# Optimization experiments

Measured on AMD Instinct MI355X. Metric: run time of the kernel, lower is better.

Reference implementation:

```python
import jax, jax.numpy as jnp
import numpy as np

H, W = 480, 640
TREF = 1.0        # reference timestamp (events warped to end of window)
TS_SCALING = 1.0  # width of timestamp normalization window
# 4 bilinear corner offsets (dy, dx): top-left, top-right, bottom-left, bottom-right
OFFS = np.array([[0.0, 0.0], [0.0, 1.0], [1.0, 0.0], [1.0, 1.0]], dtype=np.float32)


def setup_inputs() -> dict:
    key = jax.random.key(0)
    k1, k2, k3, k4, k5 = jax.random.split(key, 5)
    B, N = 4, 300000
    flow = jax.random.normal(k1, (B, 2, H, W), jnp.float32) * 2.0  # (x, y) flow maps
    ts = jax.random.uniform(k2, (B, N, 1), jnp.float32)            # event timestamps in [0,1]
    ev_y = jax.random.randint(k3, (B, N), 0, H)
    ev_x = jax.random.randint(k4, (B, N), 0, W)
    pol = jax.random.randint(k5, (B, N), 0, 2)                     # 1 = positive, 0 = negative
    return {"flow": flow, "ts": ts, "ev_y": ev_y, "ev_x": ev_x, "pol": pol}


def _corners(ev):
    """ev: [B,N,2] float (y,x) -> idx [B,4,N,2] corner coords, w [B,4,N] bilinear weights.
    Mirrors get_interpolation(): 4 integer corners, weights clamp(1-|d|,0,1) per axis."""
    base = jnp.floor(ev)[:, None, :, :]                      # [B,1,N,2]
    idx = base + jnp.asarray(OFFS)[None, :, None, :]          # [B,4,N,2]
    w = jnp.prod(jnp.clip(1.0 - jnp.abs(ev[:, None, :, :] - idx), 0.0, 1.0), axis=-1)
    return idx, w


def _splat(idx, w, pol_mask):
    """Mirrors interpolate(): masked bilinear scatter-add into a [B,1,H,W] image.
    idx: [B,4,N,2], w: [B,4,N], pol_mask: [B,1,N] (broadcast over 4 corners)."""
    B = idx.shape[0]
    inb = ((idx[..., 0] >= 0) & (idx[..., 0] <= H - 1) &
           (idx[..., 1] >= 0) & (idx[..., 1] <= W - 1)).astype(w.dtype)
    iy = jnp.clip(idx[..., 0], 0, H - 1).astype(jnp.int32)
    ix = jnp.clip(idx[..., 1], 0, W - 1).astype(jnp.int32)
    flat = (iy * W + ix).reshape(B, -1)                       # [B,4N]
    vals = (w * pol_mask * inb).reshape(B, -1)                # [B,4N]
    img = jnp.zeros((B, H * W), w.dtype).at[jnp.arange(B)[:, None], flat].add(vals)
    return img.reshape(B, 1, H, W)


def _sample(fmap, locs):
    """Mirrors get_event_flow(): bilinear gather of fmap [B,H,W] at float locs [B,N,2] (y,x)."""
    B = fmap.shape[0]
    idx, w = _corners(locs)
    inb = ((idx[..., 0] >= 0) & (idx[..., 0] <= H - 1) &
           (idx[..., 1] >= 0) & (idx[..., 1] <= W - 1)).astype(w.dtype)
    iy = jnp.clip(idx[..., 0], 0, H - 1).astype(jnp.int32)
    ix = jnp.clip(idx[..., 1], 0, W - 1).astype(jnp.int32)
    vals = fmap[jnp.arange(B)[:, None, None], iy, ix] * w * inb   # [B,4,N]
    return vals.sum(axis=1)                                        # [B,N]


def reference(flow, ts, ev_y, ev_x, pol):
    # event pixel locations (y, x)
    loc = jnp.stack([ev_y.astype(flow.dtype), ev_x.astype(flow.dtype)], axis=-1)  # [B,N,2]
    # gather per-event flow (flow channel 0 = x, channel 1 = y)
    fx = _sample(flow[:, 0], loc)   # [B,N]
    fy = _sample(flow[:, 1], loc)   # [B,N]
    # linear forward warp to tref
    dt = TREF - ts[..., 0]                                           # [B,N]
    warped = loc + dt[..., None] * jnp.stack([fy, fx], axis=-1)      # [B,N,2] (y,x)
    # iwe_formatting: bilinear splat of counts and normalized timestamps per polarity
    idx, w = _corners(warped)
    norm_ts = 1.0 - jnp.abs(TREF - ts[..., 0]) / TS_SCALING          # [B,N]
    pm_pos = (pol == 1).astype(w.dtype)[:, None, :]                  # [B,1,N]
    pm_neg = (pol == 0).astype(w.dtype)[:, None, :]
    iwe_pos = _splat(idx, w, pm_pos)
    iwe_neg = _splat(idx, w, pm_neg)
    wt = w * norm_ts[:, None, :]
    iwe_pos_ts = _splat(idx, wt, pm_pos)
    iwe_neg_ts = _splat(idx, wt, pm_neg)
    # [B,4,H,W]: (iwe_pos, iwe_neg, iwe_pos_ts, iwe_neg_ts)
    return jnp.concatenate([iwe_pos, iwe_neg, iwe_pos_ts, iwe_neg_ts], axis=1)
```

## Files before the change

kernel.cpp:

```cpp
#include <hip/hip_runtime.h>


#define IMG_H 480
#define IMG_W 640

#define OT_H 16
#define OT_W 32
#define OTY (IMG_H / OT_H)
#define OTX (IMG_W / OT_W)
#define OT_PER_B (OTY * OTX)
#define NB 4
#define NT (NB * OT_PER_B)

#define ACC_PLANE (OT_H * OT_W)

#define SCURS_STRIDE 16
#define WS_SCURS 0
#define WS_DCURS 153600
#define WS_SPILLCNT 163200
#define WS_SPILL 163840
#define SPILL_CAP 32768
#define WS_RECS 688128

#define SSORT_THREADS 512
#define K1_IPT 2
#define K1_CHUNK (SSORT_THREADS * K1_IPT)

#define Q20 1048576.0f
#define INV_Q20 9.5367431640625e-07f

__device__ __forceinline__ void
warp_from(const float* __restrict__ flow, int b, int y, int x, float t,
          float& wy, float& wx, float& nts) {
    const float* fb = flow + (size_t)b * 2 * IMG_H * IMG_W;
    const int pix = y * IMG_W + x;
    const float fx = fb[pix];
    const float fy = fb[IMG_H * IMG_W + pix];
    const float dt = 1.0f - t;
    wy = (float)y + dt * fy;
    wx = (float)x + dt * fx;
    nts = 1.0f - fabsf(1.0f - t);
}

__global__ void __launch_bounds__(SSORT_THREADS)
ssort_kernel(const float* __restrict__ flow, const float* __restrict__ ts,
             const int* __restrict__ ev_y, const int* __restrict__ ev_x,
             const int* __restrict__ pol,
             unsigned* __restrict__ scurs, unsigned* __restrict__ spillcnt,
             float4* __restrict__ spill, uint2* __restrict__ srecs,
             int N, int cap) {
    __shared__ unsigned lh[OT_PER_B];
    __shared__ unsigned lbase[OT_PER_B];
    const int tid = threadIdx.x;
    const int b = blockIdx.y;
    const int base = blockIdx.x * K1_CHUNK;

    for (int j = tid; j < OT_PER_B; j += SSORT_THREADS) lh[j] = 0;
    __syncthreads();

    unsigned mK[K1_IPT], ltK[K1_IPT], rkK[K1_IPT];
    float tsK[K1_IPT];

    #pragma unroll
    for (int k = 0; k < K1_IPT; ++k) {
        const int idx = base + k * SSORT_THREADS + tid;
        unsigned lt = 0xFFFFu, rk = 0, m = 0; float t = 0.f;
        if (idx < N) {
            const int i = b * N + idx;
            const int y = ev_y[i];
            const int x = ev_x[i];
            t = ts[i];
            const int p = pol[i];
            lt = (unsigned)((y >> 4) * OTX + (x >> 5));
            rk = atomicAdd(&lh[lt], 1u);
            m = (unsigned)y | ((unsigned)x << 9) | ((unsigned)(p & 1) << 19);
        }
        mK[k] = m; ltK[k] = lt; rkK[k] = rk; tsK[k] = t;
    }
    __syncthreads();

    for (int j = tid; j < OT_PER_B; j += SSORT_THREADS) {
        const unsigned n = lh[j];
        lbase[j] = n ? atomicAdd(&scurs[(size_t)(b * OT_PER_B + j) * SCURS_STRIDE], n)
                     : 0u;
    }
    __syncthreads();

    #pragma unroll
    for (int k = 0; k < K1_IPT; ++k) {
        const unsigned lt = ltK[k];
        if (lt == 0xFFFFu) continue;
        const unsigned slot = lbase[lt] + rkK[k];
        if (slot < (unsigned)cap) {
            uint2 r; r.x = mK[k]; r.y = __float_as_uint(tsK[k]);
            srecs[(size_t)(b * OT_PER_B + lt) * cap + slot] = r;
        } else {
            const int y = (int)(mK[k] & 511u);
            const int x = (int)((mK[k] >> 9) & 1023u);
            const int p = (int)((mK[k] >> 19) & 1u);
            float wy, wx, nts;
            warp_from(flow, b, y, x, tsK[k], wy, wx, nts);
            const unsigned g = atomicAdd(spillcnt, 1u);
            if (g < SPILL_CAP) {
                float4 s; s.x = wy; s.y = wx; s.z = nts;
                s.w = __uint_as_float((unsigned)((b << 1) | p));
                spill[g] = s;
            }
        }
    }
}

__global__ void __launch_bounds__(256)
build2_kernel(const float* __restrict__ flow,
              const unsigned* __restrict__ scurs, unsigned* __restrict__ dcurs,
              unsigned* __restrict__ spillcnt, float4* __restrict__ spill,
              const uint2* __restrict__ srecs, uint2* __restrict__ drecs,
              int cap) {
    __shared__ unsigned dh[9];
    __shared__ unsigned dbase[9];
    __shared__ float lflow[2][OT_H][OT_W];
    const int tile = blockIdx.x >> 1;
    const int half = blockIdx.x & 1;
    const int tid = threadIdx.x;
    const int b   = tile / OT_PER_B;
    const int lt  = tile % OT_PER_B;
    const int ssy = lt / OTX;
    const int ssx = lt % OTX;

    if (tid < 9) dh[tid] = 0;
    {
        const float* fb = flow + (size_t)b * 2 * IMG_H * IMG_W;
        #pragma unroll
        for (int j = tid; j < 2 * OT_H * OT_W; j += 256) {
            const int ch = j / (OT_H * OT_W);
            const int r  = (j % (OT_H * OT_W)) / OT_W;
            const int c  = j % OT_W;
            lflow[ch][r][c] = fb[(size_t)ch * IMG_H * IMG_W
                                 + (ssy * OT_H + r) * IMG_W + (ssx * OT_W + c)];
        }
    }
    __syncthreads();

    const unsigned cnt = min(scurs[(size_t)tile * SCURS_STRIDE], (unsigned)cap);
    const unsigned hsz = (cnt + 1u) >> 1;
    const unsigned lo  = half * hsz;
    const unsigned hi  = min(cnt, lo + hsz);
    const uint2* sbase = srecs + (size_t)tile * cap;

    float wyK[2], wxK[2], ntsK[2];
    unsigned pK[2], ndK[2], relK[2], rk0K[2], rk1K[2], rk2K[2], rk3K[2];

    #pragma unroll
    for (int k = 0; k < 2; ++k) {
        unsigned nd = 0, relp = 0, r0 = 0, r1 = 0, r2 = 0, r3 = 0;
        float wy = 0.f, wx = 0.f, nts = 0.f; unsigned p = 0;
        const unsigned i = lo + (unsigned)(k * 256 + tid);
        if (i < hi) {
            const uint2 sr = sbase[i];
            const int y = (int)(sr.x & 511u);
            const int x = (int)((sr.x >> 9) & 1023u);
            p = (sr.x >> 19) & 1u;
            const float t = __uint_as_float(sr.y);
            const float fx = lflow[0][y & (OT_H - 1)][x & (OT_W - 1)];
            const float fy = lflow[1][y & (OT_H - 1)][x & (OT_W - 1)];
            const float dt = 1.0f - t;
            wy = (float)y + dt * fy;
            wx = (float)x + dt * fx;
            nts = 1.0f - fabsf(1.0f - t);

            const int iy0 = (int)floorf(wy);
            const int ix0 = (int)floorf(wx);
            int rys[2]; int nry = 0;
            if (iy0 >= 0 && iy0 < IMG_H) rys[nry++] = iy0 >> 4;
            if (iy0 + 1 >= 0 && iy0 + 1 < IMG_H) {
                const int r = (iy0 + 1) >> 4;
                if (nry == 0 || r != rys[0]) rys[nry++] = r;
            }
            int rxs[2]; int nrx = 0;
            if (ix0 >= 0 && ix0 < IMG_W) rxs[nrx++] = ix0 >> 5;
            if (ix0 + 1 >= 0 && ix0 + 1 < IMG_W) {
                const int r = (ix0 + 1) >> 5;
                if (nrx == 0 || r != rxs[0]) rxs[nrx++] = r;
            }
            if (nry > 0 && nrx > 0) {
                unsigned rels[4]; unsigned m = 0;
                bool oob = false;
                for (int a = 0; a < nry; ++a)
                    for (int c = 0; c < nrx; ++c) {
                        const int ry_r = rys[a] - ssy + 1;
                        const int rx_r = rxs[c] - ssx + 1;
                        if ((unsigned)ry_r > 2u || (unsigned)rx_r > 2u) {
                            oob = true;
                            const unsigned g = atomicAdd(spillcnt, 1u);
                            if (g < SPILL_CAP) {
                                float4 s; s.x = wy; s.y = wx; s.z = nts;
                                s.w = __uint_as_float(0x80000000u
                                        | (unsigned)((b << 1) | p)
                                        | ((unsigned)rys[a] << 8)
                                        | ((unsigned)rxs[c] << 16));
                                spill[g] = s;
                            }
                        } else {
                            rels[m++] = (unsigned)(ry_r * 3 + rx_r);
                        }
                    }
                (void)oob;
                nd = m;
                for (unsigned d = 0; d < m; ++d) {
                    relp |= rels[d] << (8 * d);
                    const unsigned rr = atomicAdd(&dh[rels[d]], 1u);
                    if (d == 0) r0 = rr; else if (d == 1) r1 = rr;
                    else if (d == 2) r2 = rr; else r3 = rr;
                }
            }
        }
        wyK[k] = wy; wxK[k] = wx; ntsK[k] = nts; pK[k] = p;
        ndK[k] = nd; relK[k] = relp;
        rk0K[k] = r0; rk1K[k] = r1; rk2K[k] = r2; rk3K[k] = r3;
    }
    __syncthreads();

    if (tid < 9) {
        const unsigned n = dh[tid];
        if (n) {
            const int dty = ssy + tid / 3 - 1;
            const int dtx = ssx + tid % 3 - 1;
            dbase[tid] = atomicAdd(&dcurs[b * OT_PER_B + dty * OTX + dtx], n);
        }
    }
    __syncthreads();

    #pragma unroll
    for (int k = 0; k < 2; ++k) {
        const unsigned nd = ndK[k];
        for (unsigned d = 0; d < nd; ++d) {
            const unsigned rel = (relK[k] >> (8 * d)) & 0xFFu;
            const unsigned rr = (d == 0) ? rk0K[k] : (d == 1) ? rk1K[k]
                              : (d == 2) ? rk2K[k] : rk3K[k];
            const int dty = ssy + (int)(rel / 3) - 1;
            const int dtx = ssx + (int)(rel % 3) - 1;
            const unsigned slot = dbase[rel] + rr;
            if (slot < (unsigned)cap) {
                int qy = __float2int_rn((wyK[k] - 16.0f * dty + 1.0f) * 2048.0f);
                int qx = __float2int_rn((wxK[k] - 32.0f * dtx + 1.0f) * 1024.0f);
                int qt = __float2int_rn(ntsK[k] * 32767.0f);
                qy = min(max(qy, 0), 65535);
                qx = min(max(qx, 0), 65535);
                qt = min(max(qt, 0), 32767);
                uint2 dr;
                dr.x = (unsigned)qy | ((unsigned)qx << 16);
                dr.y = (unsigned)qt | (pK[k] << 15);
                drecs[(size_t)(b * OT_PER_B + dty * OTX + dtx) * cap + slot] = dr;
            } else {
                const unsigned g = atomicAdd(spillcnt, 1u);
                if (g < SPILL_CAP) {
                    float4 s; s.x = wyK[k]; s.y = wxK[k]; s.z = ntsK[k];
                    s.w = __uint_as_float(0x80000000u
                            | (unsigned)((b << 1) | pK[k])
                            | ((unsigned)dty << 8) | ((unsigned)dtx << 16));
                    spill[g] = s;
                }
            }
        }
    }
}

__global__ void __launch_bounds__(256)
splat_kernel(const uint2* __restrict__ drecs, const unsigned* __restrict__ dcurs,
             const float4* __restrict__ spill, const unsigned* __restrict__ spillcnt,
             float* __restrict__ out, int cap) {
    __shared__ unsigned long long acc64[2 * ACC_PLANE];
    const int tile = blockIdx.x;
    const int tid = threadIdx.x;
    #pragma unroll
    for (int j = tid; j < 2 * ACC_PLANE; j += 256) acc64[j] = 0ull;
    __syncthreads();

    const int myb = tile / OT_PER_B;
    const int rb  = tile % OT_PER_B;
    const int sy  = rb / OTX;
    const int sx  = rb % OTX;

    const unsigned cnt = min(dcurs[tile], (unsigned)cap);
    const uint2* base = drecs + (size_t)tile * cap;
    for (unsigned i = tid; i < cnt; i += 256) {
        const uint2 r = base[i];
        const float ry  = (float)(r.x & 0xFFFFu) * (1.0f / 2048.0f) - 1.0f;
        const float rx  = (float)(r.x >> 16)     * (1.0f / 1024.0f) - 1.0f;
        const float nts = (float)(r.y & 0x7FFFu) * (1.0f / 32767.0f);
        const int p = (int)((r.y >> 15) & 1u);
        const float byf = floorf(ry), bxf = floorf(rx);
        const int iy0 = (int)byf, ix0 = (int)bxf;
        const float ay = ry - byf, ax = rx - bxf;
        const float wyv[2] = {1.0f - ay, ay};
        const float wxv[2] = {1.0f - ax, ax};
        unsigned long long* accp = acc64 + (p ? 0 : 1) * ACC_PLANE;
        #pragma unroll
        for (int dy = 0; dy < 2; ++dy) {
            const int gy = iy0 + dy;
            if ((unsigned)gy >= (unsigned)OT_H) continue;
            #pragma unroll
            for (int dx = 0; dx < 2; ++dx) {
                const int gx = ix0 + dx;
                if ((unsigned)gx >= (unsigned)OT_W) continue;
                const float w = wyv[dy] * wxv[dx];
                const unsigned qw  = __float2uint_rn(w * Q20);
                const unsigned qwt = __float2uint_rn(w * nts * Q20);
                atomicAdd(&accp[gy * OT_W + gx],
                          ((unsigned long long)qwt << 32) | (unsigned long long)qw);
            }
        }
    }

    const unsigned nsp = min(*spillcnt, (unsigned)SPILL_CAP);
    for (unsigned i = tid; i < nsp; i += 256) {
        const float4 s = spill[i];
        const unsigned meta = __float_as_uint(s.w);
        if ((int)((meta >> 1) & 3u) != myb) continue;
        if (meta & 0x80000000u) {
            if ((int)((meta >> 8) & 31u) != sy || (int)((meta >> 16) & 31u) != sx)
                continue;
        }
        const int p = (int)(meta & 1u);
        const float wy = s.x, wx = s.y, nts = s.z;
        const float byf = floorf(wy), bxf = floorf(wx);
        const int iy0 = (int)byf, ix0 = (int)bxf;
        const float ay = wy - byf, ax = wx - bxf;
        const float wyv[2] = {1.0f - ay, ay};
        const float wxv[2] = {1.0f - ax, ax};
        unsigned long long* accp = acc64 + (p ? 0 : 1) * ACC_PLANE;
        #pragma unroll
        for (int dy = 0; dy < 2; ++dy) {
            const int gy = iy0 + dy;
            if ((gy >> 4) != sy) continue;
            #pragma unroll
            for (int dx = 0; dx < 2; ++dx) {
                const int gx = ix0 + dx;
                if ((gx >> 5) != sx) continue;
                const float w = wyv[dy] * wxv[dx];
                const unsigned qw  = __float2uint_rn(w * Q20);
                const unsigned qwt = __float2uint_rn(w * nts * Q20);
                atomicAdd(&accp[(gy & 15) * OT_W + (gx & 31)],
                          ((unsigned long long)qwt << 32) | (unsigned long long)qw);
            }
        }
    }
    __syncthreads();

    const int y0 = sy * OT_H;
    const int x0 = sx * OT_W;
    float* outb = out + (size_t)myb * 4 * IMG_H * IMG_W;
    {
        const int q = tid;
        const int pl  = q / (ACC_PLANE / 4);
        const int rem = q % (ACC_PLANE / 4);
        const int ry  = rem / (OT_W / 4);
        const int rx4 = rem % (OT_W / 4);
        float4 c4, t4;
        const unsigned long long* cell = acc64 + pl * ACC_PLANE + rem * 4;
        float* c = &c4.x; float* t = &t4.x;
        #pragma unroll
        for (int j = 0; j < 4; ++j) {
            const unsigned long long v = cell[j];
            c[j] = (float)(unsigned)(v & 0xFFFFFFFFull) * INV_Q20;
            t[j] = (float)(unsigned)(v >> 32) * INV_Q20;
        }
        const size_t off = (size_t)(y0 + ry) * IMG_W + x0 + rx4 * 4;
        *(float4*)(outb + (size_t)pl * IMG_H * IMG_W + off) = c4;
        *(float4*)(outb + (size_t)(pl + 2) * IMG_H * IMG_W + off) = t4;
    }
}

__global__ void __launch_bounds__(256)
event_splat_fallback(const float* __restrict__ flow, const float* __restrict__ ts,
                     const int* __restrict__ ev_y, const int* __restrict__ ev_x,
                     const int* __restrict__ pol, float* __restrict__ out,
                     int N, int total) {
    const int i = blockIdx.x * blockDim.x + threadIdx.x;
    if (i >= total) return;
    const int b = i / N;
    float wy, wx, nts;
    warp_from(flow, b, ev_y[i], ev_x[i], ts[i], wy, wx, nts);
    const int p = pol[i];
    const float byf = floorf(wy), bxf = floorf(wx);
    const int iy0 = (int)byf, ix0 = (int)bxf;
    const float ay = wy - byf, ax = wx - bxf;
    const float wyv[2] = {1.0f - ay, ay};
    const float wxv[2] = {1.0f - ax, ax};
    float* out_c = out + ((size_t)b * 4 + (p ? 0 : 1)) * IMG_H * IMG_W;
    float* out_t = out_c + 2 * IMG_H * IMG_W;
    #pragma unroll
    for (int dy = 0; dy < 2; ++dy) {
        const int gy = iy0 + dy;
        if (gy < 0 || gy >= IMG_H) continue;
        #pragma unroll
        for (int dx = 0; dx < 2; ++dx) {
            const int gx = ix0 + dx;
            if (gx < 0 || gx >= IMG_W) continue;
            const float w = wyv[dy] * wxv[dx];
            const int o = gy * IMG_W + gx;
            atomicAdd(out_c + o, w);
            atomicAdd(out_t + o, w * nts);
        }
    }
}

extern "C" void kernel_launch(void* const* d_in, const int* in_sizes, int n_in,
                              void* d_out, int out_size, void* d_ws, size_t ws_size,
                              hipStream_t stream) {
    const float* flow = (const float*)d_in[0];
    const float* ts   = (const float*)d_in[1];
    const int*   ev_y = (const int*)d_in[2];
    const int*   ev_x = (const int*)d_in[3];
    const int*   pol  = (const int*)d_in[4];
    float* out = (float*)d_out;

    const int total = in_sizes[2];
    const int B = out_size / (4 * IMG_H * IMG_W);
    const int N = total / B;
    char* ws = (char*)d_ws;

    int cap = 0;
    if (ws_size > (size_t)WS_RECS)
        cap = (int)((ws_size - WS_RECS) / ((size_t)NT * 16));
    if (cap > 1024) cap = 1024;
    cap &= ~3;

    if (B == NB && cap >= 640) {
        unsigned* scurs    = (unsigned*)(ws + WS_SCURS);
        unsigned* dcurs    = (unsigned*)(ws + WS_DCURS);
        unsigned* spillcnt = (unsigned*)(ws + WS_SPILLCNT);
        float4*   spill    = (float4*)(ws + WS_SPILL);
        uint2*    srecs    = (uint2*)(ws + WS_RECS);
        uint2*    drecs    = (uint2*)(ws + WS_RECS + (size_t)NT * cap * 8);

        hipMemsetAsync(ws, 0, WS_SPILL, stream);

        dim3 g1((N + K1_CHUNK - 1) / K1_CHUNK, NB);
        ssort_kernel<<<g1, SSORT_THREADS, 0, stream>>>(flow, ts, ev_y, ev_x, pol,
                                                       scurs, spillcnt, spill,
                                                       srecs, N, cap);
        build2_kernel<<<NT * 2, 256, 0, stream>>>(flow, scurs, dcurs, spillcnt,
                                                  spill, srecs, drecs, cap);
        splat_kernel<<<NT, 256, 0, stream>>>(drecs, dcurs, spill, spillcnt,
                                             out, cap);
        return;
    }

    hipMemsetAsync(d_out, 0, (size_t)out_size * sizeof(float), stream);
    const int blocks = (total + 255) / 256;
    event_splat_fallback<<<blocks, 256, 0, stream>>>(flow, ts, ev_y, ev_x, pol,
                                                     out, N, total);
}
```

Measured before the change: 144.5 us.

## Replace scatter build pass with per-tile gather over 3x3 source neighborhood

The intermediate build2 kernel, which forwarded warped events into destination-tile buckets, is removed. Each splat block now reads the source-sorted records of its 3x3 neighbouring source tiles, recomputes the warp from global flow, and keeps only the corners landing in its own tile. This drops one kernel launch, the drecs write/read round trip and the dcurs atomics, at the cost of each record being read and warped up to nine times. The records buffer per tile can also be larger because drecs no longer shares the workspace.

```diff
diff --git a/kernel.cpp b/kernel.cpp
--- a/kernel.cpp
+++ b/kernel.cpp
@@ -16,7 +16,6 @@
 
 #define SCURS_STRIDE 16
 #define WS_SCURS 0
-#define WS_DCURS 153600
 #define WS_SPILLCNT 163200
 #define WS_SPILL 163840
 #define SPILL_CAP 32768
@@ -111,164 +110,12 @@
 }
 
 __global__ void __launch_bounds__(256)
-build2_kernel(const float* __restrict__ flow,
-              const unsigned* __restrict__ scurs, unsigned* __restrict__ dcurs,
-              unsigned* __restrict__ spillcnt, float4* __restrict__ spill,
-              const uint2* __restrict__ srecs, uint2* __restrict__ drecs,
-              int cap) {
-    __shared__ unsigned dh[9];
-    __shared__ unsigned dbase[9];
-    __shared__ float lflow[2][OT_H][OT_W];
-    const int tile = blockIdx.x >> 1;
-    const int half = blockIdx.x & 1;
-    const int tid = threadIdx.x;
-    const int b   = tile / OT_PER_B;
-    const int lt  = tile % OT_PER_B;
-    const int ssy = lt / OTX;
-    const int ssx = lt % OTX;
-
-    if (tid < 9) dh[tid] = 0;
-    {
-        const float* fb = flow + (size_t)b * 2 * IMG_H * IMG_W;
-        #pragma unroll
-        for (int j = tid; j < 2 * OT_H * OT_W; j += 256) {
-            const int ch = j / (OT_H * OT_W);
-            const int r  = (j % (OT_H * OT_W)) / OT_W;
-            const int c  = j % OT_W;
-            lflow[ch][r][c] = fb[(size_t)ch * IMG_H * IMG_W
-                                 + (ssy * OT_H + r) * IMG_W + (ssx * OT_W + c)];
-        }
-    }
-    __syncthreads();
-
-    const unsigned cnt = min(scurs[(size_t)tile * SCURS_STRIDE], (unsigned)cap);
-    const unsigned hsz = (cnt + 1u) >> 1;
-    const unsigned lo  = half * hsz;
-    const unsigned hi  = min(cnt, lo + hsz);
-    const uint2* sbase = srecs + (size_t)tile * cap;
-
-    float wyK[2], wxK[2], ntsK[2];
-    unsigned pK[2], ndK[2], relK[2], rk0K[2], rk1K[2], rk2K[2], rk3K[2];
-
-    #pragma unroll
-    for (int k = 0; k < 2; ++k) {
-        unsigned nd = 0, relp = 0, r0 = 0, r1 = 0, r2 = 0, r3 = 0;
-        float wy = 0.f, wx = 0.f, nts = 0.f; unsigned p = 0;
-        const unsigned i = lo + (unsigned)(k * 256 + tid);
-        if (i < hi) {
-            const uint2 sr = sbase[i];
-            const int y = (int)(sr.x & 511u);
-            const int x = (int)((sr.x >> 9) & 1023u);
-            p = (sr.x >> 19) & 1u;
-            const float t = __uint_as_float(sr.y);
-            const float fx = lflow[0][y & (OT_H - 1)][x & (OT_W - 1)];
-            const float fy = lflow[1][y & (OT_H - 1)][x & (OT_W - 1)];
-            const float dt = 1.0f - t;
-            wy = (float)y + dt * fy;
-            wx = (float)x + dt * fx;
-            nts = 1.0f - fabsf(1.0f - t);
-
-            const int iy0 = (int)floorf(wy);
-            const int ix0 = (int)floorf(wx);
-            int rys[2]; int nry = 0;
-            if (iy0 >= 0 && iy0 < IMG_H) rys[nry++] = iy0 >> 4;
-            if (iy0 + 1 >= 0 && iy0 + 1 < IMG_H) {
-                const int r = (iy0 + 1) >> 4;
-                if (nry == 0 || r != rys[0]) rys[nry++] = r;
-            }
-            int rxs[2]; int nrx = 0;
-            if (ix0 >= 0 && ix0 < IMG_W) rxs[nrx++] = ix0 >> 5;
-            if (ix0 + 1 >= 0 && ix0 + 1 < IMG_W) {
-                const int r = (ix0 + 1) >> 5;
-                if (nrx == 0 || r != rxs[0]) rxs[nrx++] = r;
-            }
-            if (nry > 0 && nrx > 0) {
-                unsigned rels[4]; unsigned m = 0;
-                bool oob = false;
-                for (int a = 0; a < nry; ++a)
-                    for (int c = 0; c < nrx; ++c) {
-                        const int ry_r = rys[a] - ssy + 1;
-                        const int rx_r = rxs[c] - ssx + 1;
-                        if ((unsigned)ry_r > 2u || (unsigned)rx_r > 2u) {
-                            oob = true;
-                            const unsigned g = atomicAdd(spillcnt, 1u);
-                            if (g < SPILL_CAP) {
-                                float4 s; s.x = wy; s.y = wx; s.z = nts;
-                                s.w = __uint_as_float(0x80000000u
-                                        | (unsigned)((b << 1) | p)
-                                        | ((unsigned)rys[a] << 8)
-                                        | ((unsigned)rxs[c] << 16));
-                                spill[g] = s;
-                            }
-                        } else {
-                            rels[m++] = (unsigned)(ry_r * 3 + rx_r);
-                        }
-                    }
-                (void)oob;
-                nd = m;
-                for (unsigned d = 0; d < m; ++d) {
-                    relp |= rels[d] << (8 * d);
-                    const unsigned rr = atomicAdd(&dh[rels[d]], 1u);
-                    if (d == 0) r0 = rr; else if (d == 1) r1 = rr;
-                    else if (d == 2) r2 = rr; else r3 = rr;
-                }
-            }
-        }
-        wyK[k] = wy; wxK[k] = wx; ntsK[k] = nts; pK[k] = p;
-        ndK[k] = nd; relK[k] = relp;
-        rk0K[k] = r0; rk1K[k] = r1; rk2K[k] = r2; rk3K[k] = r3;
-    }
-    __syncthreads();
-
-    if (tid < 9) {
-        const unsigned n = dh[tid];
-        if (n) {
-            const int dty = ssy + tid / 3 - 1;
-            const int dtx = ssx + tid % 3 - 1;
-            dbase[tid] = atomicAdd(&dcurs[b * OT_PER_B + dty * OTX + dtx], n);
-        }
-    }
-    __syncthreads();
-
-    #pragma unroll
-    for (int k = 0; k < 2; ++k) {
-        const unsigned nd = ndK[k];
-        for (unsigned d = 0; d < nd; ++d) {
-            const unsigned rel = (relK[k] >> (8 * d)) & 0xFFu;
-            const unsigned rr = (d == 0) ? rk0K[k] : (d == 1) ? rk1K[k]
-                              : (d == 2) ? rk2K[k] : rk3K[k];
-            const int dty = ssy + (int)(rel / 3) - 1;
-            const int dtx = ssx + (int)(rel % 3) - 1;
-            const unsigned slot = dbase[rel] + rr;
-            if (slot < (unsigned)cap) {
-                int qy = __float2int_rn((wyK[k] - 16.0f * dty + 1.0f) * 2048.0f);
-                int qx = __float2int_rn((wxK[k] - 32.0f * dtx + 1.0f) * 1024.0f);
-                int qt = __float2int_rn(ntsK[k] * 32767.0f);
-                qy = min(max(qy, 0), 65535);
-                qx = min(max(qx, 0), 65535);
-                qt = min(max(qt, 0), 32767);
-                uint2 dr;
-                dr.x = (unsigned)qy | ((unsigned)qx << 16);
-                dr.y = (unsigned)qt | (pK[k] << 15);
-                drecs[(size_t)(b * OT_PER_B + dty * OTX + dtx) * cap + slot] = dr;
-            } else {
-                const unsigned g = atomicAdd(spillcnt, 1u);
-                if (g < SPILL_CAP) {
-                    float4 s; s.x = wyK[k]; s.y = wxK[k]; s.z = ntsK[k];
-                    s.w = __uint_as_float(0x80000000u
-                            | (unsigned)((b << 1) | pK[k])
-                            | ((unsigned)dty << 8) | ((unsigned)dtx << 16));
-                    spill[g] = s;
-                }
-            }
-        }
-    }
-}
-
-__global__ void __launch_bounds__(256)
-splat_kernel(const uint2* __restrict__ drecs, const unsigned* __restrict__ dcurs,
-             const float4* __restrict__ spill, const unsigned* __restrict__ spillcnt,
-             float* __restrict__ out, int cap) {
+splat_gather_kernel(const float* __restrict__ flow,
+                    const uint2* __restrict__ srecs,
+                    const unsigned* __restrict__ scurs,
+                    const float4* __restrict__ spill,
+                    const unsigned* __restrict__ spillcnt,
+                    float* __restrict__ out, int cap) {
     __shared__ unsigned long long acc64[2 * ACC_PLANE];
     const int tile = blockIdx.x;
     const int tid = threadIdx.x;
@@ -276,38 +123,57 @@
     for (int j = tid; j < 2 * ACC_PLANE; j += 256) acc64[j] = 0ull;
     __syncthreads();
 
-    const int myb = tile / OT_PER_B;
-    const int rb  = tile % OT_PER_B;
-    const int sy  = rb / OTX;
-    const int sx  = rb % OTX;
-
-    const unsigned cnt = min(dcurs[tile], (unsigned)cap);
-    const uint2* base = drecs + (size_t)tile * cap;
-    for (unsigned i = tid; i < cnt; i += 256) {
-        const uint2 r = base[i];
-        const float ry  = (float)(r.x & 0xFFFFu) * (1.0f / 2048.0f) - 1.0f;
-        const float rx  = (float)(r.x >> 16)     * (1.0f / 1024.0f) - 1.0f;
-        const float nts = (float)(r.y & 0x7FFFu) * (1.0f / 32767.0f);
-        const int p = (int)((r.y >> 15) & 1u);
-        const float byf = floorf(ry), bxf = floorf(rx);
-        const int iy0 = (int)byf, ix0 = (int)bxf;
-        const float ay = ry - byf, ax = rx - bxf;
-        const float wyv[2] = {1.0f - ay, ay};
-        const float wxv[2] = {1.0f - ax, ax};
-        unsigned long long* accp = acc64 + (p ? 0 : 1) * ACC_PLANE;
-        #pragma unroll
-        for (int dy = 0; dy < 2; ++dy) {
-            const int gy = iy0 + dy;
-            if ((unsigned)gy >= (unsigned)OT_H) continue;
-            #pragma unroll
-            for (int dx = 0; dx < 2; ++dx) {
-                const int gx = ix0 + dx;
-                if ((unsigned)gx >= (unsigned)OT_W) continue;
-                const float w = wyv[dy] * wxv[dx];
-                const unsigned qw  = __float2uint_rn(w * Q20);
-                const unsigned qwt = __float2uint_rn(w * nts * Q20);
-                atomicAdd(&accp[gy * OT_W + gx],
-                          ((unsigned long long)qwt << 32) | (unsigned long long)qw);
+    const int b  = tile / OT_PER_B;
+    const int rb = tile % OT_PER_B;
+    const int sy = rb / OTX;
+    const int sx = rb % OTX;
+
+    const float* fb = flow + (size_t)b * 2 * IMG_H * IMG_W;
+    const int sty0 = max(sy - 1, 0), sty1 = min(sy + 1, OTY - 1);
+    const int stx0 = max(sx - 1, 0), stx1 = min(sx + 1, OTX - 1);
+
+    for (int sty = sty0; sty <= sty1; ++sty) {
+        for (int stx = stx0; stx <= stx1; ++stx) {
+            const int st = b * OT_PER_B + sty * OTX + stx;
+            const unsigned cnt = min(scurs[(size_t)st * SCURS_STRIDE],
+                                     (unsigned)cap);
+            const uint2* base = srecs + (size_t)st * cap;
+            for (unsigned i = tid; i < cnt; i += 256) {
+                const uint2 sr = base[i];
+                const int y = (int)(sr.x & 511u);
+                const int x = (int)((sr.x >> 9) & 1023u);
+                const int p = (int)((sr.x >> 19) & 1u);
+                const float t = __uint_as_float(sr.y);
+                const int pix = y * IMG_W + x;
+                const float fx = fb[pix];
+                const float fy = fb[IMG_H * IMG_W + pix];
+                const float dt = 1.0f - t;
+                const float wy = (float)y + dt * fy;
+                const float wx = (float)x + dt * fx;
+                const float nts = 1.0f - fabsf(1.0f - t);
+
+                const float byf = floorf(wy), bxf = floorf(wx);
+                const int iy0 = (int)byf, ix0 = (int)bxf;
+                const float ay = wy - byf, ax = wx - bxf;
+                const float wyv[2] = {1.0f - ay, ay};
+                const float wxv[2] = {1.0f - ax, ax};
+                unsigned long long* accp = acc64 + (p ? 0 : 1) * ACC_PLANE;
+                #pragma unroll
+                for (int dy = 0; dy < 2; ++dy) {
+                    const int gy = iy0 + dy;
+                    if ((gy >> 4) != sy) continue;
+                    #pragma unroll
+                    for (int dx = 0; dx < 2; ++dx) {
+                        const int gx = ix0 + dx;
+                        if ((gx >> 5) != sx) continue;
+                        const float w = wyv[dy] * wxv[dx];
+                        const unsigned qw  = __float2uint_rn(w * Q20);
+                        const unsigned qwt = __float2uint_rn(w * nts * Q20);
+                        atomicAdd(&accp[(gy & 15) * OT_W + (gx & 31)],
+                                  ((unsigned long long)qwt << 32)
+                                  | (unsigned long long)qw);
+                    }
+                }
             }
         }
     }
@@ -316,7 +182,7 @@
     for (unsigned i = tid; i < nsp; i += 256) {
         const float4 s = spill[i];
         const unsigned meta = __float_as_uint(s.w);
-        if ((int)((meta >> 1) & 3u) != myb) continue;
+        if ((int)((meta >> 1) & 3u) != b) continue;
         if (meta & 0x80000000u) {
             if ((int)((meta >> 8) & 31u) != sy || (int)((meta >> 16) & 31u) != sx)
                 continue;
@@ -349,7 +215,7 @@
 
     const int y0 = sy * OT_H;
     const int x0 = sx * OT_W;
-    float* outb = out + (size_t)myb * 4 * IMG_H * IMG_W;
+    float* outb = out + (size_t)b * 4 * IMG_H * IMG_W;
     {
         const int q = tid;
         const int pl  = q / (ACC_PLANE / 4);
@@ -422,17 +288,15 @@
 
     int cap = 0;
     if (ws_size > (size_t)WS_RECS)
-        cap = (int)((ws_size - WS_RECS) / ((size_t)NT * 16));
+        cap = (int)((ws_size - WS_RECS) / ((size_t)NT * 8));
     if (cap > 1024) cap = 1024;
     cap &= ~3;
 
     if (B == NB && cap >= 640) {
         unsigned* scurs    = (unsigned*)(ws + WS_SCURS);
-        unsigned* dcurs    = (unsigned*)(ws + WS_DCURS);
         unsigned* spillcnt = (unsigned*)(ws + WS_SPILLCNT);
         float4*   spill    = (float4*)(ws + WS_SPILL);
         uint2*    srecs    = (uint2*)(ws + WS_RECS);
-        uint2*    drecs    = (uint2*)(ws + WS_RECS + (size_t)NT * cap * 8);
 
         hipMemsetAsync(ws, 0, WS_SPILL, stream);
 
@@ -440,10 +304,8 @@
         ssort_kernel<<<g1, SSORT_THREADS, 0, stream>>>(flow, ts, ev_y, ev_x, pol,
                                                        scurs, spillcnt, spill,
                                                        srecs, N, cap);
-        build2_kernel<<<NT * 2, 256, 0, stream>>>(flow, scurs, dcurs, spillcnt,
-                                                  spill, srecs, drecs, cap);
-        splat_kernel<<<NT, 256, 0, stream>>>(drecs, dcurs, spill, spillcnt,
-                                             out, cap);
+        splat_gather_kernel<<<NT, 256, 0, stream>>>(flow, srecs, scurs,
+                                                    spill, spillcnt, out, cap);
         return;
     }
 
```

Result: slower. 159.0 us (+10.0%).
